# Kernel tuning notes

Hardware: AMD Instinct MI355X
Metric: run time of the kernel (lower is better)

The kernel has to match this reference:

```python
import jax, jax.numpy as jnp
import numpy as np

D_MODEL = 1024
HEADS = 16
D_K = D_MODEL // HEADS
D_FF = 4096
B, S = 2, 2048
EPS = 1e-5


def setup_inputs() -> dict:
    key = jax.random.key(0)
    ks = jax.random.split(key, 16)
    sc_att = 1.0 / np.sqrt(D_MODEL)
    sc_ff1 = 1.0 / np.sqrt(D_MODEL)
    sc_ff2 = 1.0 / np.sqrt(D_FF)
    return {
        "input": jax.random.normal(ks[0], (B, S, D_MODEL), jnp.float32),
        "mask": jnp.ones((B, 1, 1, S), jnp.int32),
        # stacked per-head projections: [H, D_MODEL, D_K]
        "Wq": jax.random.normal(ks[1], (HEADS, D_MODEL, D_K), jnp.float32) * sc_att,
        "bq": jax.random.normal(ks[2], (HEADS, D_K), jnp.float32) * 0.01,
        "Wk": jax.random.normal(ks[3], (HEADS, D_MODEL, D_K), jnp.float32) * sc_att,
        "bk": jax.random.normal(ks[4], (HEADS, D_K), jnp.float32) * 0.01,
        "Wv": jax.random.normal(ks[5], (HEADS, D_MODEL, D_K), jnp.float32) * sc_att,
        "bv": jax.random.normal(ks[6], (HEADS, D_K), jnp.float32) * 0.01,
        "Wo": jax.random.normal(ks[7], (D_MODEL, D_MODEL), jnp.float32) * sc_att,
        "bo": jax.random.normal(ks[8], (D_MODEL,), jnp.float32) * 0.01,
        "ln1_g": jnp.ones((D_MODEL,), jnp.float32),
        "ln1_b": jnp.zeros((D_MODEL,), jnp.float32),
        "ln2_g": jnp.ones((D_MODEL,), jnp.float32),
        "ln2_b": jnp.zeros((D_MODEL,), jnp.float32),
        "W1": jax.random.normal(ks[9], (D_MODEL, D_FF), jnp.float32) * sc_ff1,
        "b1": jax.random.normal(ks[10], (D_FF,), jnp.float32) * 0.01,
        "W2": jax.random.normal(ks[11], (D_FF, D_MODEL), jnp.float32) * sc_ff2,
        "b2": jax.random.normal(ks[12], (D_MODEL,), jnp.float32) * 0.01,
    }


def _layernorm(x, g, b):
    mu = jnp.mean(x, axis=-1, keepdims=True)
    var = jnp.mean(jnp.square(x - mu), axis=-1, keepdims=True)
    return (x - mu) * jax.lax.rsqrt(var + EPS) * g + b


def reference(input, mask, Wq, bq, Wk, bk, Wv, bv, Wo, bo,
              ln1_g, ln1_b, ln2_g, ln2_b, W1, b1, W2, b2):
    x = input
    # per-head projections, stacked: [B,H,S,D_K]
    q = jnp.einsum('bsd,hdk->bhsk', x, Wq) + bq[None, :, None, :]
    k = jnp.einsum('bsd,hdk->bhsk', x, Wk) + bk[None, :, None, :]
    v = jnp.einsum('bsd,hdk->bhsk', x, Wv) + bv[None, :, None, :]
    scores = jnp.einsum('bhqk,bhsk->bhqs', q, k) / np.sqrt(D_K)  # [B,H,S,S]
    scores = jnp.where(mask == 0, jnp.float32(-1e9), scores)
    attn = jax.nn.softmax(scores, axis=-1)
    ctx = jnp.einsum('bhqs,bhsk->bhqk', attn, v)  # [B,H,S,D_K]
    # concat heads along feature dim (head h occupies slice h*D_K:(h+1)*D_K)
    ctx = jnp.transpose(ctx, (0, 2, 1, 3)).reshape(B, S, D_MODEL)
    att_out = ctx @ Wo + bo
    h = _layernorm(x + att_out, ln1_g, ln1_b)
    ff = jax.nn.relu(h @ W1 + b1) @ W2 + b2
    return _layernorm(h + ff, ln2_g, ln2_b)
```

## Files before the change

kernel.cpp:

```cpp
#include <hip/hip_runtime.h>
#include <cstdint>
#include <cstddef>

typedef unsigned short u16;
typedef unsigned int   u32;
typedef unsigned short u16x4 __attribute__((ext_vector_type(4)));
typedef unsigned short u16x8 __attribute__((ext_vector_type(8)));
typedef unsigned int   u32x2 __attribute__((ext_vector_type(2)));
typedef __bf16 bf16x8 __attribute__((ext_vector_type(8)));
typedef float f32x4 __attribute__((ext_vector_type(4)));

#define MFMA16(a, b, c) __builtin_amdgcn_mfma_f32_16x16x32_bf16((a), (b), (c), 0, 0, 0)

__device__ __forceinline__ float bf2f(u16 h) {
  union { unsigned u; float f; } v; v.u = ((unsigned)h) << 16; return v.f;
}
__device__ __forceinline__ u16 f2bf(float f) {
  union { float f; unsigned u; } v; v.f = f;
  unsigned r = v.u + 0x7fffu + ((v.u >> 16) & 1u);
  return (u16)(r >> 16);
}
__device__ __forceinline__ void gll16(const u16* g, u16* l) {
  __builtin_amdgcn_global_load_lds(
      (const __attribute__((address_space(1))) void*)g,
      (__attribute__((address_space(3))) void*)l, 16, 0, 0);
}

__global__ __launch_bounds__(256) void transpose_qkv(
    const float* __restrict__ Wq, const float* __restrict__ Wk,
    const float* __restrict__ Wv, u16* __restrict__ outb) {
  __shared__ u16 tile[32][33];
  const int z = blockIdx.z;
  const int which = z >> 4, h = z & 15;
  const float* in = (which == 0 ? Wq : (which == 1 ? Wk : Wv)) + (size_t)h * 1024 * 64;
  u16* out = outb + ((size_t)which * 1024 + h * 64) * 1024;
  const int tx = threadIdx.x & 31, ty = threadIdx.x >> 5;
  const int r0 = blockIdx.y * 32, c0 = blockIdx.x * 32;
  #pragma unroll
  for (int i = 0; i < 32; i += 8)
    tile[ty + i][tx] = f2bf(in[(size_t)(r0 + ty + i) * 64 + c0 + tx]);
  __syncthreads();
  #pragma unroll
  for (int i = 0; i < 32; i += 8)
    out[(size_t)(c0 + ty + i) * 1024 + r0 + tx] = tile[tx][ty + i];
}

__global__ __launch_bounds__(256) void transpose_any(
    const float* __restrict__ in, u16* __restrict__ out, int R, int C) {
  __shared__ u16 tile[32][33];
  const int tx = threadIdx.x & 31, ty = threadIdx.x >> 5;
  const int r0 = blockIdx.y * 32, c0 = blockIdx.x * 32;
  #pragma unroll
  for (int i = 0; i < 32; i += 8)
    tile[ty + i][tx] = f2bf(in[(size_t)(r0 + ty + i) * C + c0 + tx]);
  __syncthreads();
  #pragma unroll
  for (int i = 0; i < 32; i += 8)
    out[(size_t)(c0 + ty + i) * R + r0 + tx] = tile[tx][ty + i];
}

__global__ __launch_bounds__(256) void cat_bias(
    const float* __restrict__ bq, const float* __restrict__ bk,
    const float* __restrict__ bv, float* __restrict__ o) {
  int i = blockIdx.x * 256 + threadIdx.x;
  if (i >= 3072) return;
  o[i] = (i < 1024) ? bq[i] : (i < 2048 ? bk[i - 1024] : bv[i - 2048]);
}

__global__ __launch_bounds__(256) void prep_madd(
    const int* __restrict__ mask, float* __restrict__ madd) {
  int i = blockIdx.x * 256 + threadIdx.x;
  if (i >= 4096) return;
  madd[i] = mask[i] ? -16.0f : -1.0e9f;
}

__global__ __launch_bounds__(256) void cvt_x(
    const float* __restrict__ in, u16* __restrict__ out, int n) {
  int i = (blockIdx.x * 256 + threadIdx.x) * 4;
  if (i >= n) return;
  const float4 v = *(const float4*)&in[i];
  u16x4 o;
  o[0] = f2bf(v.x); o[1] = f2bf(v.y); o[2] = f2bf(v.z); o[3] = f2bf(v.w);
  *(u16x4*)&out[i] = o;
}

template <int MODE>
__global__ __launch_bounds__(256) void gemm_bt(
    const u16* __restrict__ A, const u16* __restrict__ Bt,
    const float* __restrict__ bias, u16* __restrict__ C,
    int M, int N, int K) {
  __shared__ __align__(16) u16 As[2][128 * 32];
  __shared__ __align__(16) u16 Bs[2][128 * 32];
  const int tid = threadIdx.x;
  const int lane = tid & 63;
  const int wave = tid >> 6;
  const int m0 = blockIdx.y * 128;
  const int n0 = blockIdx.x * 128;
  const int wr = (wave >> 1) * 64;
  const int wc = (wave & 1) * 64;
  const int lrow = lane & 15;
  const int quad = lane >> 4;

  const int srow = lane >> 2;
  const int scol = (lane & 3) * 8;
  const u16* gA1 = &A[(size_t)(m0 + wave * 16 + srow) * K + scol];
  const u16* gA2 = &A[(size_t)(m0 + 64 + wave * 16 + srow) * K + scol];
  const u16* gB1 = &Bt[(size_t)(n0 + wave * 16 + srow) * K + scol];
  const u16* gB2 = &Bt[(size_t)(n0 + 64 + wave * 16 + srow) * K + scol];
  const int so1 = (wave * 16) * 32;
  const int so2 = (wave * 16 + 64) * 32;

  f32x4 acc[4][4];
  #pragma unroll
  for (int i = 0; i < 4; ++i)
    #pragma unroll
    for (int j = 0; j < 4; ++j)
      acc[i][j] = (f32x4){0.f, 0.f, 0.f, 0.f};

  for (int k0 = 0; k0 < K; k0 += 64) {
    gll16(gA1 + k0, &As[0][so1]);
    gll16(gA2 + k0, &As[0][so2]);
    gll16(gB1 + k0, &Bs[0][so1]);
    gll16(gB2 + k0, &Bs[0][so2]);
    gll16(gA1 + k0 + 32, &As[1][so1]);
    gll16(gA2 + k0 + 32, &As[1][so2]);
    gll16(gB1 + k0 + 32, &Bs[1][so1]);
    gll16(gB2 + k0 + 32, &Bs[1][so2]);
    __syncthreads();
    #pragma unroll
    for (int kb = 0; kb < 2; ++kb) {
      bf16x8 af[4], bfr[4];
      #pragma unroll
      for (int i = 0; i < 4; ++i) {
        af[i]  = *(const bf16x8*)&As[kb][(wr + i * 16 + lrow) * 32 + quad * 8];
        bfr[i] = *(const bf16x8*)&Bs[kb][(wc + i * 16 + lrow) * 32 + quad * 8];
      }
      #pragma unroll
      for (int fr = 0; fr < 4; ++fr)
        #pragma unroll
        for (int fc = 0; fc < 4; ++fc)
          acc[fr][fc] = MFMA16(af[fr], bfr[fc], acc[fr][fc]);
    }
    __syncthreads();
  }

  #pragma unroll
  for (int fr = 0; fr < 4; ++fr) {
    int rowb = m0 + wr + fr * 16 + quad * 4;
    #pragma unroll
    for (int fc = 0; fc < 4; ++fc) {
      int col = n0 + wc + fc * 16 + lrow;
      float bv = bias[col];
      #pragma unroll
      for (int r = 0; r < 4; ++r) {
        float v = acc[fr][fc][r] + bv;
        if (MODE == 1) v = fmaxf(v, 0.f);
        C[(size_t)(rowb + r) * N + col] = f2bf(v);
      }
    }
  }
}

__global__ __launch_bounds__(256) void gemm64_bt(
    const u16* __restrict__ A, const u16* __restrict__ Bt,
    const float* __restrict__ bias, u16* __restrict__ C,
    int M, int N, int K) {
  __shared__ __align__(16) u16 As[2][64 * 32];
  __shared__ __align__(16) u16 Bs[2][128 * 32];
  const int tid = threadIdx.x;
  const int lane = tid & 63;
  const int wave = tid >> 6;
  const int m0 = blockIdx.y * 64;
  const int n0 = blockIdx.x * 128;
  const int wr = (wave >> 1) * 32;
  const int wc = (wave & 1) * 64;
  const int lrow = lane & 15;
  const int quad = lane >> 4;

  const int srow = lane >> 2;
  const int scol = (lane & 3) * 8;
  const u16* gA1 = &A[(size_t)(m0 + wave * 16 + srow) * K + scol];
  const u16* gB1 = &Bt[(size_t)(n0 + wave * 16 + srow) * K + scol];
  const u16* gB2 = &Bt[(size_t)(n0 + 64 + wave * 16 + srow) * K + scol];
  const int so1 = (wave * 16) * 32;
  const int so2 = (wave * 16 + 64) * 32;

  f32x4 acc[2][4];
  #pragma unroll
  for (int i = 0; i < 2; ++i)
    #pragma unroll
    for (int j = 0; j < 4; ++j)
      acc[i][j] = (f32x4){0.f, 0.f, 0.f, 0.f};

  for (int k0 = 0; k0 < K; k0 += 64) {
    gll16(gA1 + k0, &As[0][so1]);
    gll16(gB1 + k0, &Bs[0][so1]);
    gll16(gB2 + k0, &Bs[0][so2]);
    gll16(gA1 + k0 + 32, &As[1][so1]);
    gll16(gB1 + k0 + 32, &Bs[1][so1]);
    gll16(gB2 + k0 + 32, &Bs[1][so2]);
    __syncthreads();
    #pragma unroll
    for (int kb = 0; kb < 2; ++kb) {
      bf16x8 af[2], bfr[4];
      #pragma unroll
      for (int i = 0; i < 2; ++i)
        af[i] = *(const bf16x8*)&As[kb][(wr + i * 16 + lrow) * 32 + quad * 8];
      #pragma unroll
      for (int j = 0; j < 4; ++j)
        bfr[j] = *(const bf16x8*)&Bs[kb][(wc + j * 16 + lrow) * 32 + quad * 8];
      #pragma unroll
      for (int fr = 0; fr < 2; ++fr)
        #pragma unroll
        for (int fc = 0; fc < 4; ++fc)
          acc[fr][fc] = MFMA16(af[fr], bfr[fc], acc[fr][fc]);
    }
    __syncthreads();
  }

  #pragma unroll
  for (int fr = 0; fr < 2; ++fr) {
    int rowb = m0 + wr + fr * 16 + quad * 4;
    #pragma unroll
    for (int fc = 0; fc < 4; ++fc) {
      int col = n0 + wc + fc * 16 + lrow;
      float bv = bias[col];
      #pragma unroll
      for (int r = 0; r < 4; ++r) {
        float v = acc[fr][fc][r] + bv;
        C[(size_t)(rowb + r) * N + col] = f2bf(v);
      }
    }
  }
}

__global__ __launch_bounds__(256) void attn_kernel(
    const u16* __restrict__ xqkv, const float* __restrict__ madd,
    u16* __restrict__ ctx) {
  __shared__ __align__(16) u16 Ks[64][72];
  __shared__ __align__(16) u16 Vt[64][136];
  __shared__ __align__(16) u16 Ps[4][2][16][72];
  const int tid = threadIdx.x;
  const int lane = tid & 63;
  const int wave = tid >> 6;
  const int lrow = lane & 15;
  const int quad = lane >> 4;
  const int b = blockIdx.z, h = blockIdx.y;
  const int qb = blockIdx.x * 128 + wave * 16;
  const u16* Qp = xqkv + (size_t)b * 2048 * 3072 + h * 64;
  const u16* Kp = Qp + 1024;
  const u16* Vp = Qp + 2048;

  bf16x8 qa[2][2];
  #pragma unroll
  for (int t = 0; t < 2; ++t) {
    qa[t][0] = *(const bf16x8*)&Qp[(size_t)(qb + t * 64 + lrow) * 3072 + quad * 8];
    qa[t][1] = *(const bf16x8*)&Qp[(size_t)(qb + t * 64 + lrow) * 3072 + 32 + quad * 8];
  }

  f32x4 o[2][4];
  #pragma unroll
  for (int t = 0; t < 2; ++t)
    #pragma unroll
    for (int i = 0; i < 4; ++i) o[t][i] = (f32x4){0.f, 0.f, 0.f, 0.f};
  float rsum[2] = {0.f, 0.f};

  const int ks_row = tid >> 3, ks_col = (tid & 7) * 8;
  const int v_dg = tid >> 4;
  const int v_kp = tid & 15;
  const float* maddb = madd + b * 2048;

  u16x8 kreg[2];
  u16x4 va[2], vb[2];
  #pragma unroll
  for (int sh = 0; sh < 2; ++sh) {
    kreg[sh] = *(const u16x8*)&Kp[(size_t)(sh * 32 + ks_row) * 3072 + ks_col];
    va[sh] = *(const u16x4*)&Vp[(size_t)(sh * 32 + 2 * v_kp) * 3072 + v_dg * 4];
    vb[sh] = *(const u16x4*)&Vp[(size_t)(sh * 32 + 2 * v_kp + 1) * 3072 + v_dg * 4];
  }

  for (int s0 = 0; s0 < 2048; s0 += 64) {
    __syncthreads();
    #pragma unroll
    for (int sh = 0; sh < 2; ++sh) {
      *(u16x8*)&Ks[sh * 32 + ks_row][ks_col] = kreg[sh];
      #pragma unroll
      for (int j = 0; j < 4; ++j) {
        u32 pk = ((u32)vb[sh][j] << 16) | (u32)va[sh][j];
        *(u32*)&Vt[v_dg * 4 + j][sh * 32 + 2 * v_kp] = pk;
      }
    }
    __syncthreads();
    if (s0 + 64 < 2048) {
      #pragma unroll
      for (int sh = 0; sh < 2; ++sh) {
        int sb = s0 + 64 + sh * 32;
        kreg[sh] = *(const u16x8*)&Kp[(size_t)(sb + ks_row) * 3072 + ks_col];
        va[sh] = *(const u16x4*)&Vp[(size_t)(sb + 2 * v_kp) * 3072 + v_dg * 4];
        vb[sh] = *(const u16x4*)&Vp[(size_t)(sb + 2 * v_kp + 1) * 3072 + v_dg * 4];
      }
    }

    bf16x8 kf[4][2], vf[4][2];
    #pragma unroll
    for (int kb = 0; kb < 4; ++kb) {
      kf[kb][0] = *(const bf16x8*)&Ks[kb * 16 + lrow][quad * 8];
      kf[kb][1] = *(const bf16x8*)&Ks[kb * 16 + lrow][32 + quad * 8];
    }
    #pragma unroll
    for (int nb = 0; nb < 4; ++nb) {
      vf[nb][0] = *(const bf16x8*)&Vt[nb * 16 + lrow][quad * 8];
      vf[nb][1] = *(const bf16x8*)&Vt[nb * 16 + lrow][32 + quad * 8];
    }

    #pragma unroll
    for (int t = 0; t < 2; ++t) {
      #pragma unroll
      for (int kb = 0; kb < 4; ++kb) {
        f32x4 z = (f32x4){0.f, 0.f, 0.f, 0.f};
        z = MFMA16(kf[kb][0], qa[t][0], z);
        z = MFMA16(kf[kb][1], qa[t][1], z);
        f32x4 m4 = *(const f32x4*)&maddb[s0 + kb * 16 + quad * 4];
        u32 pb[4];
        #pragma unroll
        for (int r = 0; r < 4; ++r) {
          float p = __expf(z[r] * 0.125f + m4[r]);
          rsum[t] += p;
          union { float f; u32 u; } cv; cv.f = p;
          pb[r] = cv.u + 0x8000u;
        }
        u32x2 w2;
        w2[0] = __builtin_amdgcn_perm(pb[1], pb[0], 0x07060302);
        w2[1] = __builtin_amdgcn_perm(pb[3], pb[2], 0x07060302);
        *(u32x2*)&Ps[wave][t][lrow][kb * 16 + quad * 4] = w2;
      }
      #pragma unroll
      for (int kh = 0; kh < 2; ++kh) {
        bf16x8 pa = *(const bf16x8*)&Ps[wave][t][lrow][kh * 32 + quad * 8];
        #pragma unroll
        for (int nb = 0; nb < 4; ++nb)
          o[t][nb] = MFMA16(pa, vf[nb][kh], o[t][nb]);
      }
    }
  }

  #pragma unroll
  for (int t = 0; t < 2; ++t) {
    float rs = rsum[t];
    rs += __shfl_xor(rs, 16, 64);
    rs += __shfl_xor(rs, 32, 64);
    float inv = 1.f / fmaxf(rs, 1e-30f);
    #pragma unroll
    for (int r = 0; r < 4; ++r) {
      float invq = __shfl(inv, quad * 4 + r, 64);
      int q = qb + t * 64 + quad * 4 + r;
      #pragma unroll
      for (int nb = 0; nb < 4; ++nb) {
        float v = o[t][nb][r] * invq;
        ctx[((size_t)b * 2048 + q) * 1024 + h * 64 + nb * 16 + lrow] = f2bf(v);
      }
    }
  }
}

template <int IN_BF, int OUT_BF>
__global__ __launch_bounds__(256) void add_ln(
    const void* __restrict__ xa_, const u16* __restrict__ ya,
    const float* __restrict__ g, const float* __restrict__ bb,
    void* __restrict__ outp_) {
  __shared__ float red[8];
  const int tid = threadIdx.x;
  const size_t base = (size_t)blockIdx.x * 1024;
  const float* xf = (const float*)xa_;
  const u16*   xb = (const u16*)xa_;
  float v[4];
  float s = 0.f;
  #pragma unroll
  for (int i = 0; i < 4; ++i) {
    int c = i * 256 + tid;
    float xv = IN_BF ? bf2f(xb[base + c]) : xf[base + c];
    v[i] = xv + bf2f(ya[base + c]);
    s += v[i];
  }
  #pragma unroll
  for (int off = 32; off > 0; off >>= 1) s += __shfl_down(s, off, 64);
  if ((tid & 63) == 0) red[tid >> 6] = s;
  __syncthreads();
  float mean = (red[0] + red[1] + red[2] + red[3]) * (1.f / 1024.f);
  float s2 = 0.f;
  #pragma unroll
  for (int i = 0; i < 4; ++i) { float d = v[i] - mean; s2 += d * d; }
  #pragma unroll
  for (int off = 32; off > 0; off >>= 1) s2 += __shfl_down(s2, off, 64);
  if ((tid & 63) == 0) red[4 + (tid >> 6)] = s2;
  __syncthreads();
  float var = (red[4] + red[5] + red[6] + red[7]) * (1.f / 1024.f);
  float rstd = rsqrtf(var + 1e-5f);
  #pragma unroll
  for (int i = 0; i < 4; ++i) {
    int c = i * 256 + tid;
    float r = (v[i] - mean) * rstd * g[c] + bb[c];
    if (OUT_BF) ((u16*)outp_)[base + c] = f2bf(r);
    else        ((float*)outp_)[base + c] = r;
  }
}

extern "C" void kernel_launch(void* const* d_in, const int* in_sizes, int n_in,
                              void* d_out, int out_size, void* d_ws, size_t ws_size,
                              hipStream_t stream) {
  (void)in_sizes; (void)n_in; (void)out_size; (void)ws_size;
  const float* x    = (const float*)d_in[0];
  const int*   mask = (const int*)d_in[1];
  const float* Wq   = (const float*)d_in[2];
  const float* bq   = (const float*)d_in[3];
  const float* Wk   = (const float*)d_in[4];
  const float* bk   = (const float*)d_in[5];
  const float* Wv   = (const float*)d_in[6];
  const float* bv   = (const float*)d_in[7];
  const float* Wo   = (const float*)d_in[8];
  const float* bo   = (const float*)d_in[9];
  const float* ln1g = (const float*)d_in[10];
  const float* ln1b = (const float*)d_in[11];
  const float* ln2g = (const float*)d_in[12];
  const float* ln2b = (const float*)d_in[13];
  const float* W1   = (const float*)d_in[14];
  const float* b1   = (const float*)d_in[15];
  const float* W2   = (const float*)d_in[16];
  const float* b2   = (const float*)d_in[17];
  float* out = (float*)d_out;

  char* ws = (char*)d_ws;
  u16*   Wqkv_t = (u16*)(ws + 0);
  u16*   W1_t   = (u16*)(ws + 0);
  u16*   Wo_t   = (u16*)(ws + 8388608);
  u16*   W2_t   = (u16*)(ws + 8388608);
  u16*   xb     = (u16*)(ws + 16777216);
  u16*   xqkv   = (u16*)(ws + 25165824);
  u16*   ctx    = (u16*)(ws + 50331648);
  u16*   ff1    = (u16*)(ws + 25165824);
  u16*   attout = (u16*)(ws + 58720256);
  u16*   ff2    = attout;
  u16*   hbuf   = (u16*)(ws + 67108864);
  float* biasq  = (float*)(ws + 75497472);
  float* maddg  = (float*)(ws + 75509760);

  transpose_qkv<<<dim3(2, 32, 48), 256, 0, stream>>>(Wq, Wk, Wv, Wqkv_t);
  transpose_any<<<dim3(32, 32), 256, 0, stream>>>(Wo, Wo_t, 1024, 1024);
  cat_bias<<<12, 256, 0, stream>>>(bq, bk, bv, biasq);
  prep_madd<<<16, 256, 0, stream>>>(mask, maddg);
  cvt_x<<<4096, 256, 0, stream>>>(x, xb, 4194304);

  gemm_bt<0><<<dim3(24, 32), 256, 0, stream>>>(xb, Wqkv_t, biasq, xqkv, 4096, 3072, 1024);
  transpose_any<<<dim3(128, 32), 256, 0, stream>>>(W1, W1_t, 1024, 4096);

  attn_kernel<<<dim3(16, 16, 2), 256, 0, stream>>>(xqkv, maddg, ctx);
  gemm64_bt<<<dim3(8, 64), 256, 0, stream>>>(ctx, Wo_t, bo, attout, 4096, 1024, 1024);
  transpose_any<<<dim3(32, 128), 256, 0, stream>>>(W2, W2_t, 4096, 1024);

  add_ln<0, 1><<<4096, 256, 0, stream>>>(x, attout, ln1g, ln1b, hbuf);
  gemm_bt<1><<<dim3(32, 32), 256, 0, stream>>>(hbuf, W1_t, b1, ff1, 4096, 4096, 1024);
  gemm64_bt<<<dim3(8, 64), 256, 0, stream>>>(ff1, W2_t, b2, ff2, 4096, 1024, 4096);
  add_ln<1, 0><<<4096, 256, 0, stream>>>(hbuf, ff2, ln2g, ln2b, out);
}
```

Baseline: 395.2 us.

## Fuse x conversion into QKV GEMM, merge prep and transpose launches, use exp2

The QKV GEMM now reads fp32 input directly and converts it to bf16 while staging into LDS, which removes the separate cvt_x kernel and its bf16 buffer. The three weight transposes become one launch, and the bias and mask prep kernels are merged into another, with the workspace laid out again so the transposed weights no longer alias each other. Softmax now uses exp2 with log2e folded into the scale and the mask offsets. Staging A through registers instead of the direct global-to-LDS load adds register pressure and VALU work inside the GEMM main loop.

Result: slower. 406.2 us (+2.8%).

```diff
diff --git a/kernel.cpp b/kernel.cpp
--- a/kernel.cpp
+++ b/kernel.cpp
@@ -7,6 +7,7 @@
 typedef unsigned short u16x4 __attribute__((ext_vector_type(4)));
 typedef unsigned short u16x8 __attribute__((ext_vector_type(8)));
 typedef unsigned int   u32x2 __attribute__((ext_vector_type(2)));
+typedef unsigned int   u32x4 __attribute__((ext_vector_type(4)));
 typedef __bf16 bf16x8 __attribute__((ext_vector_type(8)));
 typedef float f32x4 __attribute__((ext_vector_type(4)));
 
@@ -20,10 +21,31 @@
   unsigned r = v.u + 0x7fffu + ((v.u >> 16) & 1u);
   return (u16)(r >> 16);
 }
+__device__ __forceinline__ u32 pack2(float a, float b) {
+  union { float f; u32 u; } ua, ub; ua.f = a; ub.f = b;
+  u32 ra = ua.u + 0x7fffu + ((ua.u >> 16) & 1u);
+  u32 rb = ub.u + 0x7fffu + ((ub.u >> 16) & 1u);
+  return __builtin_amdgcn_perm(rb, ra, 0x07060302);
+}
 __device__ __forceinline__ void gll16(const u16* g, u16* l) {
   __builtin_amdgcn_global_load_lds(
       (const __attribute__((address_space(1))) void*)g,
       (__attribute__((address_space(3))) void*)l, 16, 0, 0);
+}
+__device__ __forceinline__ float fast_exp2(float x) {
+#if __has_builtin(__builtin_amdgcn_exp2f)
+  return __builtin_amdgcn_exp2f(x);
+#else
+  return exp2f(x);
+#endif
+}
+__device__ __forceinline__ void stage8(const float* g, u16* l) {
+  float4 u = *(const float4*)g;
+  float4 w = *(const float4*)(g + 4);
+  u32x4 q;
+  q[0] = pack2(u.x, u.y); q[1] = pack2(u.z, u.w);
+  q[2] = pack2(w.x, w.y); q[3] = pack2(w.z, w.w);
+  *(u32x4*)l = q;
 }
 
 __global__ __launch_bounds__(256) void transpose_qkv(
@@ -45,50 +67,45 @@
     out[(size_t)(c0 + ty + i) * 1024 + r0 + tx] = tile[tx][ty + i];
 }
 
-__global__ __launch_bounds__(256) void transpose_any(
-    const float* __restrict__ in, u16* __restrict__ out, int R, int C) {
+__global__ __launch_bounds__(256) void transpose_w(
+    const float* __restrict__ Wo, const float* __restrict__ W1,
+    const float* __restrict__ W2, u16* __restrict__ Wo_t,
+    u16* __restrict__ W1_t, u16* __restrict__ W2_t) {
   __shared__ u16 tile[32][33];
+  const int id = blockIdx.x;
+  const float* in; u16* outp; int R, C, cx, ry;
+  if (id < 1024)      { in = Wo; outp = Wo_t; R = 1024; C = 1024; cx = id & 31;  ry = id >> 5; }
+  else if (id < 5120) { int t = id - 1024; in = W1; outp = W1_t; R = 1024; C = 4096; cx = t & 127; ry = t >> 7; }
+  else                { int t = id - 5120; in = W2; outp = W2_t; R = 4096; C = 1024; cx = t & 31;  ry = t >> 5; }
   const int tx = threadIdx.x & 31, ty = threadIdx.x >> 5;
-  const int r0 = blockIdx.y * 32, c0 = blockIdx.x * 32;
+  const int r0 = ry * 32, c0 = cx * 32;
   #pragma unroll
   for (int i = 0; i < 32; i += 8)
     tile[ty + i][tx] = f2bf(in[(size_t)(r0 + ty + i) * C + c0 + tx]);
   __syncthreads();
   #pragma unroll
   for (int i = 0; i < 32; i += 8)
-    out[(size_t)(c0 + ty + i) * R + r0 + tx] = tile[tx][ty + i];
-}
-
-__global__ __launch_bounds__(256) void cat_bias(
+    outp[(size_t)(c0 + ty + i) * R + r0 + tx] = tile[tx][ty + i];
+}
+
+__global__ __launch_bounds__(256) void prep_small(
     const float* __restrict__ bq, const float* __restrict__ bk,
-    const float* __restrict__ bv, float* __restrict__ o) {
+    const float* __restrict__ bv, const int* __restrict__ mask,
+    float* __restrict__ biasq, float* __restrict__ madd2) {
   int i = blockIdx.x * 256 + threadIdx.x;
-  if (i >= 3072) return;
-  o[i] = (i < 1024) ? bq[i] : (i < 2048 ? bk[i - 1024] : bv[i - 2048]);
-}
-
-__global__ __launch_bounds__(256) void prep_madd(
-    const int* __restrict__ mask, float* __restrict__ madd) {
-  int i = blockIdx.x * 256 + threadIdx.x;
-  if (i >= 4096) return;
-  madd[i] = mask[i] ? -16.0f : -1.0e9f;
-}
-
-__global__ __launch_bounds__(256) void cvt_x(
-    const float* __restrict__ in, u16* __restrict__ out, int n) {
-  int i = (blockIdx.x * 256 + threadIdx.x) * 4;
-  if (i >= n) return;
-  const float4 v = *(const float4*)&in[i];
-  u16x4 o;
-  o[0] = f2bf(v.x); o[1] = f2bf(v.y); o[2] = f2bf(v.z); o[3] = f2bf(v.w);
-  *(u16x4*)&out[i] = o;
-}
-
-template <int MODE>
+  if (i < 3072) {
+    biasq[i] = (i < 1024) ? bq[i] : (i < 2048 ? bk[i - 1024] : bv[i - 2048]);
+  } else if (i < 7168) {
+    int j = i - 3072;
+    madd2[j] = mask[j] ? -23.083120f : -1.442695e9f;
+  }
+}
+
+template <int MODE, int AF32>
 __global__ __launch_bounds__(256) void gemm_bt(
-    const u16* __restrict__ A, const u16* __restrict__ Bt,
-    const float* __restrict__ bias, u16* __restrict__ C,
-    int M, int N, int K) {
+    const u16* __restrict__ A, const float* __restrict__ Af,
+    const u16* __restrict__ Bt, const float* __restrict__ bias,
+    u16* __restrict__ C, int M, int N, int K) {
   __shared__ __align__(16) u16 As[2][128 * 32];
   __shared__ __align__(16) u16 Bs[2][128 * 32];
   const int tid = threadIdx.x;
@@ -103,10 +120,19 @@
 
   const int srow = lane >> 2;
   const int scol = (lane & 3) * 8;
-  const u16* gA1 = &A[(size_t)(m0 + wave * 16 + srow) * K + scol];
-  const u16* gA2 = &A[(size_t)(m0 + 64 + wave * 16 + srow) * K + scol];
+  const u16 *gA1 = nullptr, *gA2 = nullptr;
+  const float *fA1 = nullptr, *fA2 = nullptr;
+  if (AF32) {
+    fA1 = &Af[(size_t)(m0 + wave * 16 + srow) * K + scol];
+    fA2 = &Af[(size_t)(m0 + 64 + wave * 16 + srow) * K + scol];
+  } else {
+    gA1 = &A[(size_t)(m0 + wave * 16 + srow) * K + scol];
+    gA2 = &A[(size_t)(m0 + 64 + wave * 16 + srow) * K + scol];
+  }
   const u16* gB1 = &Bt[(size_t)(n0 + wave * 16 + srow) * K + scol];
   const u16* gB2 = &Bt[(size_t)(n0 + 64 + wave * 16 + srow) * K + scol];
+  const int soA1 = (wave * 16 + srow) * 32 + scol;
+  const int soA2 = (wave * 16 + 64 + srow) * 32 + scol;
   const int so1 = (wave * 16) * 32;
   const int so2 = (wave * 16 + 64) * 32;
 
@@ -118,12 +144,19 @@
       acc[i][j] = (f32x4){0.f, 0.f, 0.f, 0.f};
 
   for (int k0 = 0; k0 < K; k0 += 64) {
-    gll16(gA1 + k0, &As[0][so1]);
-    gll16(gA2 + k0, &As[0][so2]);
+    if (AF32) {
+      stage8(fA1 + k0,      &As[0][soA1]);
+      stage8(fA2 + k0,      &As[0][soA2]);
+      stage8(fA1 + k0 + 32, &As[1][soA1]);
+      stage8(fA2 + k0 + 32, &As[1][soA2]);
+    } else {
+      gll16(gA1 + k0, &As[0][so1]);
+      gll16(gA2 + k0, &As[0][so2]);
+      gll16(gA1 + k0 + 32, &As[1][so1]);
+      gll16(gA2 + k0 + 32, &As[1][so2]);
+    }
     gll16(gB1 + k0, &Bs[0][so1]);
     gll16(gB2 + k0, &Bs[0][so2]);
-    gll16(gA1 + k0 + 32, &As[1][so1]);
-    gll16(gA2 + k0 + 32, &As[1][so2]);
     gll16(gB1 + k0 + 32, &Bs[1][so1]);
     gll16(gB2 + k0 + 32, &Bs[1][so2]);
     __syncthreads();
@@ -235,7 +268,7 @@
 }
 
 __global__ __launch_bounds__(256) void attn_kernel(
-    const u16* __restrict__ xqkv, const float* __restrict__ madd,
+    const u16* __restrict__ xqkv, const float* __restrict__ madd2,
     u16* __restrict__ ctx) {
   __shared__ __align__(16) u16 Ks[64][72];
   __shared__ __align__(16) u16 Vt[64][136];
@@ -250,6 +283,7 @@
   const u16* Qp = xqkv + (size_t)b * 2048 * 3072 + h * 64;
   const u16* Kp = Qp + 1024;
   const u16* Vp = Qp + 2048;
+  const float S2 = 0.18033688f;
 
   bf16x8 qa[2][2];
   #pragma unroll
@@ -268,7 +302,7 @@
   const int ks_row = tid >> 3, ks_col = (tid & 7) * 8;
   const int v_dg = tid >> 4;
   const int v_kp = tid & 15;
-  const float* maddb = madd + b * 2048;
+  const float* maddb = madd2 + b * 2048;
 
   u16x8 kreg[2];
   u16x4 va[2], vb[2];
@@ -324,7 +358,7 @@
         u32 pb[4];
         #pragma unroll
         for (int r = 0; r < 4; ++r) {
-          float p = __expf(z[r] * 0.125f + m4[r]);
+          float p = fast_exp2(fmaf(z[r], S2, m4[r]));
           rsum[t] += p;
           union { float f; u32 u; } cv; cv.f = p;
           pb[r] = cv.u + 0x8000u;
@@ -431,10 +465,9 @@
 
   char* ws = (char*)d_ws;
   u16*   Wqkv_t = (u16*)(ws + 0);
-  u16*   W1_t   = (u16*)(ws + 0);
-  u16*   Wo_t   = (u16*)(ws + 8388608);
-  u16*   W2_t   = (u16*)(ws + 8388608);
-  u16*   xb     = (u16*)(ws + 16777216);
+  u16*   Wo_t   = (u16*)(ws + 6291456);
+  u16*   W1_t   = (u16*)(ws + 8388608);
+  u16*   W2_t   = (u16*)(ws + 16777216);
   u16*   xqkv   = (u16*)(ws + 25165824);
   u16*   ctx    = (u16*)(ws + 50331648);
   u16*   ff1    = (u16*)(ws + 25165824);
@@ -442,23 +475,19 @@
   u16*   ff2    = attout;
   u16*   hbuf   = (u16*)(ws + 67108864);
   float* biasq  = (float*)(ws + 75497472);
-  float* maddg  = (float*)(ws + 75509760);
-
+  float* madd2  = (float*)(ws + 75509760);
+
+  prep_small<<<28, 256, 0, stream>>>(bq, bk, bv, mask, biasq, madd2);
   transpose_qkv<<<dim3(2, 32, 48), 256, 0, stream>>>(Wq, Wk, Wv, Wqkv_t);
-  transpose_any<<<dim3(32, 32), 256, 0, stream>>>(Wo, Wo_t, 1024, 1024);
-  cat_bias<<<12, 256, 0, stream>>>(bq, bk, bv, biasq);
-  prep_madd<<<16, 256, 0, stream>>>(mask, maddg);
-  cvt_x<<<4096, 256, 0, stream>>>(x, xb, 4194304);
-
-  gemm_bt<0><<<dim3(24, 32), 256, 0, stream>>>(xb, Wqkv_t, biasq, xqkv, 4096, 3072, 1024);
-  transpose_any<<<dim3(128, 32), 256, 0, stream>>>(W1, W1_t, 1024, 4096);
-
-  attn_kernel<<<dim3(16, 16, 2), 256, 0, stream>>>(xqkv, maddg, ctx);
+  transpose_w<<<9216, 256, 0, stream>>>(Wo, W1, W2, Wo_t, W1_t, W2_t);
+
+  gemm_bt<0, 1><<<dim3(24, 32), 256, 0, stream>>>(nullptr, x, Wqkv_t, biasq,
+                                                  xqkv, 4096, 3072, 1024);
+  attn_kernel<<<dim3(16, 16, 2), 256, 0, stream>>>(xqkv, madd2, ctx);
   gemm64_bt<<<dim3(8, 64), 256, 0, stream>>>(ctx, Wo_t, bo, attout, 4096, 1024, 1024);
-  transpose_any<<<dim3(32, 128), 256, 0, stream>>>(W2, W2_t, 4096, 1024);
-
   add_ln<0, 1><<<4096, 256, 0, stream>>>(x, attout, ln1g, ln1b, hbuf);
-  gemm_bt<1><<<dim3(32, 32), 256, 0, stream>>>(hbuf, W1_t, b1, ff1, 4096, 4096, 1024);
+  gemm_bt<1, 0><<<dim3(32, 32), 256, 0, stream>>>(hbuf, nullptr, W1_t, b1,
+                                                  ff1, 4096, 4096, 1024);
   gemm64_bt<<<dim3(8, 64), 256, 0, stream>>>(ff1, W2_t, b2, ff2, 4096, 1024, 4096);
   add_ln<1, 0><<<4096, 256, 0, stream>>>(hbuf, ff2, ln2g, ln2b, out);
 }
```
